# Performance work log

Measured on AMD Instinct MI355X. Metric: run time of the kernel, lower is better.

## Reference

```python
import jax, jax.numpy as jnp
import numpy as np
import math

INPUT_DIM = 256
HIDDEN_DIM = 128  # per-head dim
NUM_HEAD = 8
N = 1024          # seq len == variables
BATCH = 8
C = HIDDEN_DIM * NUM_HEAD  # 1024


def setup_inputs() -> dict:
    key = jax.random.key(0)
    ks = jax.random.split(key, 11)
    s = 0.02
    return {
        "x": jax.random.normal(ks[0], (BATCH, N, INPUT_DIM), dtype=jnp.float32),
        "B_bias": jax.random.normal(ks[1], (N, N), dtype=jnp.float32),
        "wq_w": jax.random.normal(ks[2], (INPUT_DIM, C), dtype=jnp.float32) * s,
        "wq_b": jax.random.normal(ks[3], (C,), dtype=jnp.float32) * s,
        "wk_w": jax.random.normal(ks[4], (INPUT_DIM, C), dtype=jnp.float32) * s,
        "wk_b": jax.random.normal(ks[5], (C,), dtype=jnp.float32) * s,
        "wv_w": jax.random.normal(ks[6], (INPUT_DIM, C), dtype=jnp.float32) * s,
        "wv_b": jax.random.normal(ks[7], (C,), dtype=jnp.float32) * s,
        "proj_w": jax.random.normal(ks[8], (C, HIDDEN_DIM), dtype=jnp.float32) * s,
        "proj_b": jax.random.normal(ks[9], (HIDDEN_DIM,), dtype=jnp.float32) * s,
    }


def reference(x, B_bias, wq_w, wq_b, wk_w, wk_b, wv_w, wv_b, proj_w, proj_b):
    B, n, _ = x.shape
    sdk = jnp.float32(math.sqrt(HIDDEN_DIM))
    # projections -> [B, N, C], split heads -> [B, H, N, h]
    def heads(y):
        return y.reshape(B, n, NUM_HEAD, HIDDEN_DIM).transpose(0, 2, 1, 3)
    q = heads(x @ wq_w + wq_b)
    k = heads(x @ wk_w + wk_b)
    v = heads(x @ wv_w + wv_b)
    # scores [B, H, N, N] with learned additive bias (broadcast over B, H)
    scores = jnp.einsum("bhnd,bhmd->bhnm", q, k) / sdk + B_bias
    attn = jax.nn.softmax(scores, axis=-1)
    out = jnp.einsum("bhnm,bhmd->bhnd", attn, v)  # [B, H, N, h]
    out = out.transpose(0, 2, 1, 3).reshape(B, n, C)
    return out @ proj_w + proj_b
```

## Files before the change

### kernel.cpp

```cpp
#include <hip/hip_runtime.h>
#include <math.h>

#define SEQ  1024
#define IND  256
#define CC   1024
#define NH   8
#define HD   128
#define BH   64

typedef __bf16 bf16x8 __attribute__((ext_vector_type(8)));
typedef __bf16 bf16x4 __attribute__((ext_vector_type(4)));
typedef float  f32x4  __attribute__((ext_vector_type(4)));
typedef unsigned short u16;

static constexpr float RSDK = 0.08838834764831845f;

__device__ __forceinline__ u16 f2bf(float f) {
    unsigned int u = __float_as_uint(f);
    u += 0x7fffu + ((u >> 16) & 1u);
    return (u16)(u >> 16);
}

__device__ __forceinline__ unsigned cvt_pk_bf16(float lo, float hi) {
    unsigned r;
    asm("v_cvt_pk_bf16_f32 %0, %1, %2" : "=v"(r) : "v"(lo), "v"(hi));
    return r;
}

__global__ __launch_bounds__(256) void prep_kernel(
    const float* __restrict__ x, u16* __restrict__ xb,
    const float* __restrict__ w0, const float* __restrict__ w1, const float* __restrict__ w2,
    u16* __restrict__ o0, u16* __restrict__ o1, u16* __restrict__ o2,
    const float* __restrict__ pw, u16* __restrict__ pT)
{
    __shared__ float tile[32][33];
    const int id = blockIdx.x;

    if (id < 2048) {
        const int i = id * 256 + threadIdx.x;
        float4 v = ((const float4*)x)[i];
        ushort4 o;
        o.x = f2bf(v.x); o.y = f2bf(v.y); o.z = f2bf(v.z); o.w = f2bf(v.w);
        ((ushort4*)xb)[i] = o;
        return;
    }

    const float* in; u16* out; int R, C, c0, r0;
    if (id < 2816) {
        const int rem = id - 2048;
        const int z = rem >> 8;
        const int rem2 = rem & 255;
        in  = (z == 0) ? w0 : (z == 1) ? w1 : w2;
        out = (z == 0) ? o0 : (z == 1) ? o1 : o2;
        R = IND; C = CC;
        c0 = (rem2 & 31) * 32;
        r0 = (rem2 >> 5) * 32;
    } else {
        const int rem = id - 2816;
        in = pw; out = pT;
        R = CC; C = HD;
        c0 = (rem & 3) * 32;
        r0 = (rem >> 2) * 32;
    }

    const int row = threadIdx.x >> 3, col4 = (threadIdx.x & 7) * 4;
    float4 v = *(const float4*)&in[(size_t)(r0 + row) * C + c0 + col4];
    tile[row][col4 + 0] = v.x; tile[row][col4 + 1] = v.y;
    tile[row][col4 + 2] = v.z; tile[row][col4 + 3] = v.w;
    __syncthreads();
    ushort4 o;
    o.x = f2bf(tile[col4 + 0][row]);
    o.y = f2bf(tile[col4 + 1][row]);
    o.z = f2bf(tile[col4 + 2][row]);
    o.w = f2bf(tile[col4 + 3][row]);
    *(ushort4*)&out[(size_t)(c0 + row) * R + r0 + col4] = o;
}

#define QKV_LDW 72
__global__ __launch_bounds__(256) void qkv_kernel(
    const u16* __restrict__ xb,
    const u16* __restrict__ wT0, const u16* __restrict__ wT1, const u16* __restrict__ wT2,
    const float* __restrict__ b0, const float* __restrict__ b1, const float* __restrict__ b2,
    u16* __restrict__ q_out, u16* __restrict__ k_out, u16* __restrict__ vt_out)
{
    const int mat = blockIdx.z;
    const u16* wT  = (mat == 0) ? wT0 : (mat == 1) ? wT1 : wT2;
    const float* wb = (mat == 0) ? b0 : (mat == 1) ? b1 : b2;
    const float scale = (mat == 0) ? RSDK : 1.0f;

    __shared__ __align__(16) u16 As[128 * QKV_LDW];
    __shared__ __align__(16) u16 Bs[128 * QKV_LDW];

    const int tid = threadIdx.x;
    const int lane = tid & 63, wave = tid >> 6;
    const int ln = lane & 15, quad = lane >> 4;
    const int m0 = blockIdx.x * 128;
    const int n0 = blockIdx.y * 128;
    const int wm = (wave & 1) * 64;
    const int wn = (wave >> 1) * 64;

    f32x4 acc[4][4];
    #pragma unroll
    for (int mb = 0; mb < 4; ++mb)
        #pragma unroll
        for (int nb = 0; nb < 4; ++nb)
            #pragma unroll
            for (int r = 0; r < 4; ++r) acc[mb][nb][r] = 0.0f;

    const int r8 = tid >> 3, pb8 = tid & 7;

    const u16* ag = xb + (size_t)(m0 + r8) * IND + pb8 * 8;
    const u16* bg = wT + (size_t)(n0 + r8) * IND + pb8 * 8;

    bf16x8 pa[4], pbv[4];
    #pragma unroll
    for (int c = 0; c < 4; ++c) {
        pa[c]  = *(const bf16x8*)(ag + (size_t)c * 32 * IND);
        pbv[c] = *(const bf16x8*)(bg + (size_t)c * 32 * IND);
    }

    for (int kt = 0; kt < 4; ++kt) {
        __syncthreads();
        #pragma unroll
        for (int c = 0; c < 4; ++c) {
            *(bf16x8*)(As + (size_t)(c * 32 + r8) * QKV_LDW + pb8 * 8) = pa[c];
            *(bf16x8*)(Bs + (size_t)(c * 32 + r8) * QKV_LDW + pb8 * 8) = pbv[c];
        }
        __syncthreads();
        if (kt < 3) {
            #pragma unroll
            for (int c = 0; c < 4; ++c) {
                pa[c]  = *(const bf16x8*)(ag + (size_t)c * 32 * IND + (kt + 1) * 64);
                pbv[c] = *(const bf16x8*)(bg + (size_t)c * 32 * IND + (kt + 1) * 64);
            }
        }
        #pragma unroll
        for (int ks = 0; ks < 2; ++ks) {
            bf16x8 af[4], bf[4];
            #pragma unroll
            for (int mb = 0; mb < 4; ++mb)
                af[mb] = *(const bf16x8*)(As + (size_t)(wm + mb * 16 + ln) * QKV_LDW
                                             + (ks * 4 + quad) * 8);
            #pragma unroll
            for (int nb = 0; nb < 4; ++nb)
                bf[nb] = *(const bf16x8*)(Bs + (size_t)(wn + nb * 16 + ln) * QKV_LDW
                                             + (ks * 4 + quad) * 8);
            #pragma unroll
            for (int mb = 0; mb < 4; ++mb)
                #pragma unroll
                for (int nb = 0; nb < 4; ++nb)
                    acc[mb][nb] = __builtin_amdgcn_mfma_f32_16x16x32_bf16(
                        af[mb], bf[nb], acc[mb][nb], 0, 0, 0);
        }
    }

    if (mat != 2) {
        u16* outp = (mat == 0) ? q_out : k_out;
        #pragma unroll
        for (int nb = 0; nb < 4; ++nb) {
            const int c = n0 + wn + nb * 16 + ln;
            const float bv = wb[c];
            const int h = c >> 7, d = c & 127;
            #pragma unroll
            for (int mb = 0; mb < 4; ++mb) {
                #pragma unroll
                for (int r = 0; r < 4; ++r) {
                    const int m = m0 + wm + mb * 16 + quad * 4 + r;
                    const int b = m >> 10, tok = m & 1023;
                    outp[((size_t)(b * NH + h) * SEQ + tok) * HD + d] =
                        f2bf((acc[mb][nb][r] + bv) * scale);
                }
            }
        }
    } else {
        #pragma unroll
        for (int nb = 0; nb < 4; ++nb) {
            const int c = n0 + wn + nb * 16 + ln;
            const float bv = wb[c];
            const int h = c >> 7, d = c & 127;
            #pragma unroll
            for (int mb = 0; mb < 4; ++mb) {
                const int m = m0 + wm + mb * 16 + quad * 4;
                const int b = m >> 10, tok0 = m & 1023;
                ushort4 o;
                o.x = f2bf(acc[mb][nb][0] + bv);
                o.y = f2bf(acc[mb][nb][1] + bv);
                o.z = f2bf(acc[mb][nb][2] + bv);
                o.w = f2bf(acc[mb][nb][3] + bv);
                *(ushort4*)&vt_out[((size_t)(b * NH + h) * HD + d) * SEQ + tok0] = o;
            }
        }
    }
}

#define KVB    32
#define KS_LDW 136
#define VS_LDW 40
__global__ __launch_bounds__(256, 4) void attn_kernel(
    const u16* __restrict__ Q, const u16* __restrict__ K,
    const u16* __restrict__ Vt, const float* __restrict__ bias,
    u16* __restrict__ aout)
{
    __shared__ __align__(16) u16 Ks[KVB * KS_LDW];
    __shared__ __align__(16) u16 Vs[128 * VS_LDW];

    const int tid = threadIdx.x;
    const int lane = tid & 63, wave = tid >> 6;
    const int ln = lane & 15, quad = lane >> 4;
    const int bh = blockIdx.x;
    const int q0 = blockIdx.y * 64 + wave * 16;

    bf16x8 qf[4];
    {
        const u16* qp = Q + ((size_t)bh * SEQ + q0 + ln) * HD + quad * 8;
        #pragma unroll
        for (int ks = 0; ks < 4; ++ks) qf[ks] = *(const bf16x8*)(qp + ks * 32);
    }

    f32x4 Oa[8];
    #pragma unroll
    for (int db = 0; db < 8; ++db)
        #pragma unroll
        for (int r = 0; r < 4; ++r) Oa[db][r] = 0.0f;
    float l_loc = 0.0f;

    const u16* Kg0 = K  + (size_t)bh * SEQ * HD;
    const u16* Vg0 = Vt + (size_t)bh * HD * SEQ;
    const float* brow = bias + (size_t)(q0 + ln) * SEQ + quad * 4;

    const int r16 = tid >> 4, pb16 = tid & 15;
    const int r4  = tid >> 2, pb4  = tid & 3;

    const u16* kg = Kg0 + (size_t)r16 * HD + pb16 * 8;
    const u16* vg = Vg0 + (size_t)r4 * SEQ + pb4 * 8;

    bf16x8 kp[2], vp[2];
    #pragma unroll
    for (int c = 0; c < 2; ++c) {
        kp[c] = *(const bf16x8*)(kg + (size_t)c * 16 * HD);
        vp[c] = *(const bf16x8*)(vg + (size_t)c * 64 * SEQ);
    }

    float4 bpre[2];
    #pragma unroll
    for (int nb = 0; nb < 2; ++nb)
        bpre[nb] = *(const float4*)(brow + nb * 16);

    for (int kt = 0; kt < 32; ++kt) {
        __syncthreads();
        #pragma unroll
        for (int c = 0; c < 2; ++c) {
            *(bf16x8*)(Ks + (size_t)(c * 16 + r16) * KS_LDW + pb16 * 8) = kp[c];
            *(bf16x8*)(Vs + (size_t)(c * 64 + r4) * VS_LDW + pb4 * 8)   = vp[c];
        }
        __syncthreads();

        if (kt < 31) {
            #pragma unroll
            for (int c = 0; c < 2; ++c) {
                kp[c] = *(const bf16x8*)(kg + (size_t)(kt + 1) * KVB * HD + (size_t)c * 16 * HD);
                vp[c] = *(const bf16x8*)(vg + (size_t)c * 64 * SEQ + (kt + 1) * KVB);
            }
        }

        float p8[2][4];
        #pragma unroll
        for (int nb = 0; nb < 2; ++nb) {
            const u16* kr = Ks + (size_t)(nb * 16 + ln) * KS_LDW;
            bf16x8 kf[4];
            #pragma unroll
            for (int ks = 0; ks < 4; ++ks)
                kf[ks] = *(const bf16x8*)(kr + (ks * 4 + quad) * 8);
            f32x4 s;
            #pragma unroll
            for (int r = 0; r < 4; ++r) s[r] = 0.0f;
            #pragma unroll
            for (int ks = 0; ks < 4; ++ks)
                s = __builtin_amdgcn_mfma_f32_16x16x32_bf16(kf[ks], qf[ks], s, 0, 0, 0);
            #pragma unroll
            for (int r = 0; r < 4; ++r) {
                const float p = __expf(s[r] + bpre[nb][r]);
                l_loc += p;
                p8[nb][r] = p;
            }
        }

        if (kt < 31) {
            #pragma unroll
            for (int nb = 0; nb < 2; ++nb)
                bpre[nb] = *(const float4*)(brow + (kt + 1) * KVB + nb * 16);
        }

        unsigned x0 = cvt_pk_bf16(p8[0][0], p8[0][1]);
        unsigned x1 = cvt_pk_bf16(p8[0][2], p8[0][3]);
        unsigned y0 = cvt_pk_bf16(p8[1][0], p8[1][1]);
        unsigned y1 = cvt_pk_bf16(p8[1][2], p8[1][3]);
        asm("v_permlane32_swap_b32 %0, %1" : "+v"(x0), "+v"(y0));
        asm("v_permlane32_swap_b32 %0, %1" : "+v"(x1), "+v"(y1));
        asm("v_permlane16_swap_b32 %0, %1" : "+v"(x0), "+v"(y0));
        asm("v_permlane16_swap_b32 %0, %1" : "+v"(x1), "+v"(y1));
        union { unsigned u[4]; bf16x8 v; } afu;
        afu.u[0] = x0; afu.u[1] = x1; afu.u[2] = y0; afu.u[3] = y1;
        const bf16x8 af = afu.v;

        #pragma unroll
        for (int db = 0; db < 8; ++db) {
            bf16x8 vf = *(const bf16x8*)(Vs + (size_t)(db * 16 + ln) * VS_LDW + quad * 8);
            Oa[db] = __builtin_amdgcn_mfma_f32_16x16x32_bf16(af, vf, Oa[db], 0, 0, 0);
        }
    }

    float ltot = l_loc;
    ltot += __shfl_xor(ltot, 16);
    ltot += __shfl_xor(ltot, 32);

    const int b = bh >> 3, h = bh & 7;
    #pragma unroll
    for (int r = 0; r < 4; ++r) {
        const float inv = 1.0f / __shfl(ltot, quad * 4 + r);
        const int tok = q0 + quad * 4 + r;
        u16* op = aout + ((size_t)(b * SEQ + tok)) * CC + h * HD + ln;
        #pragma unroll
        for (int db = 0; db < 8; ++db) op[db * 16] = f2bf(Oa[db][r] * inv);
    }
}

__global__ __launch_bounds__(256) void proj_kernel(
    const u16* __restrict__ A, const u16* __restrict__ pT,
    const float* __restrict__ pb, float* __restrict__ out)
{
    __shared__ float Rs[3][16 * 132];
    const int tid = threadIdx.x;
    const int lane = tid & 63, kh = tid >> 6;
    const int ln = lane & 15, quad = lane >> 4;
    const int m0 = blockIdx.x * 16;

    f32x4 acc[8];
    #pragma unroll
    for (int nb = 0; nb < 8; ++nb)
        #pragma unroll
        for (int r = 0; r < 4; ++r) acc[nb][r] = 0.0f;

    const u16* ap = A  + (size_t)(m0 + ln) * CC + kh * 256 + quad * 8;
    const u16* bp = pT + (size_t)ln * CC + kh * 256 + quad * 8;

    #pragma unroll
    for (int kt = 0; kt < 8; ++kt) {
        bf16x8 af = *(const bf16x8*)(ap + kt * 32);
        #pragma unroll
        for (int nb = 0; nb < 8; ++nb) {
            bf16x8 bf = *(const bf16x8*)(bp + (size_t)nb * 16 * CC + kt * 32);
            acc[nb] = __builtin_amdgcn_mfma_f32_16x16x32_bf16(af, bf, acc[nb], 0, 0, 0);
        }
    }

    if (kh > 0) {
        #pragma unroll
        for (int nb = 0; nb < 8; ++nb)
            #pragma unroll
            for (int r = 0; r < 4; ++r)
                Rs[kh - 1][(quad * 4 + r) * 132 + nb * 16 + ln] = acc[nb][r];
    }
    __syncthreads();
    if (kh == 0) {
        #pragma unroll
        for (int nb = 0; nb < 8; ++nb) {
            const int c = nb * 16 + ln;
            const float bv = pb[c];
            #pragma unroll
            for (int r = 0; r < 4; ++r) {
                const int ri = (quad * 4 + r) * 132 + c;
                out[(size_t)(m0 + quad * 4 + r) * HD + c] =
                    acc[nb][r] + Rs[0][ri] + Rs[1][ri] + Rs[2][ri] + bv;
            }
        }
    }
}

extern "C" void kernel_launch(void* const* d_in, const int* in_sizes, int n_in,
                              void* d_out, int out_size, void* d_ws, size_t ws_size,
                              hipStream_t stream)
{
    const float* x    = (const float*)d_in[0];
    const float* bias = (const float*)d_in[1];
    const float* wq   = (const float*)d_in[2];
    const float* wqb  = (const float*)d_in[3];
    const float* wk   = (const float*)d_in[4];
    const float* wkb  = (const float*)d_in[5];
    const float* wv   = (const float*)d_in[6];
    const float* wvb  = (const float*)d_in[7];
    const float* pw   = (const float*)d_in[8];
    const float* pb   = (const float*)d_in[9];
    float* out = (float*)d_out;

    u16* ws = (u16*)d_ws;
    size_t off = 0;
    u16* xb  = ws + off; off += (size_t)8192 * IND;
    u16* wqT = ws + off; off += (size_t)CC * IND;
    u16* wkT = ws + off; off += (size_t)CC * IND;
    u16* wvT = ws + off; off += (size_t)CC * IND;
    u16* pT  = ws + off; off += (size_t)HD * CC;
    u16* Qw  = ws + off; off += (size_t)BH * SEQ * HD;
    u16* Kw  = ws + off; off += (size_t)BH * SEQ * HD;
    u16* Vtw = ws + off; off += (size_t)BH * HD * SEQ;
    u16* Aw  = ws + off; off += (size_t)8192 * CC;

    prep_kernel<<<2944, 256, 0, stream>>>(x, xb, wq, wk, wv, wqT, wkT, wvT, pw, pT);
    qkv_kernel<<<dim3(64, 8, 3), 256, 0, stream>>>(
        xb, wqT, wkT, wvT, wqb, wkb, wvb, Qw, Kw, Vtw);
    attn_kernel<<<dim3(64, 16), 256, 0, stream>>>(Qw, Kw, Vtw, bias, Aw);
    proj_kernel<<<512, 256, 0, stream>>>(Aw, pT, pb, out);
}
```

Before: 181.8 us.

## Process two 16-row query tiles per wave in attention to reuse K/V fragments

Each wave now handles 32 query rows (two 16-row MFMA tiles) instead of 16, so every K fragment and V fragment read from LDS feeds two MFMAs. Each block covers 128 queries and the grid halves, which halves total K/V global-to-LDS traffic and the number of barrier iterations per query. The trade-off is doubled accumulator and Q registers, with launch bounds relaxed to 2 blocks per CU, plus fewer blocks (512) to spread across the GPU.

```diff
diff --git a/kernel.cpp b/kernel.cpp
--- a/kernel.cpp
+++ b/kernel.cpp
@@ -196,7 +196,7 @@
 #define KVB    32
 #define KS_LDW 136
 #define VS_LDW 40
-__global__ __launch_bounds__(256, 4) void attn_kernel(
+__global__ __launch_bounds__(256, 2) void attn_kernel(
     const u16* __restrict__ Q, const u16* __restrict__ K,
     const u16* __restrict__ Vt, const float* __restrict__ bias,
     u16* __restrict__ aout)
@@ -208,25 +208,29 @@
     const int lane = tid & 63, wave = tid >> 6;
     const int ln = lane & 15, quad = lane >> 4;
     const int bh = blockIdx.x;
-    const int q0 = blockIdx.y * 64 + wave * 16;
-
-    bf16x8 qf[4];
-    {
-        const u16* qp = Q + ((size_t)bh * SEQ + q0 + ln) * HD + quad * 8;
-        #pragma unroll
-        for (int ks = 0; ks < 4; ++ks) qf[ks] = *(const bf16x8*)(qp + ks * 32);
-    }
-
-    f32x4 Oa[8];
-    #pragma unroll
-    for (int db = 0; db < 8; ++db)
-        #pragma unroll
-        for (int r = 0; r < 4; ++r) Oa[db][r] = 0.0f;
-    float l_loc = 0.0f;
+    const int q0 = blockIdx.y * 128 + wave * 32;
+
+    bf16x8 qf[2][4];
+    #pragma unroll
+    for (int mb = 0; mb < 2; ++mb) {
+        const u16* qp = Q + ((size_t)bh * SEQ + q0 + mb * 16 + ln) * HD + quad * 8;
+        #pragma unroll
+        for (int ks = 0; ks < 4; ++ks) qf[mb][ks] = *(const bf16x8*)(qp + ks * 32);
+    }
+
+    f32x4 Oa[2][8];
+    #pragma unroll
+    for (int mb = 0; mb < 2; ++mb)
+        #pragma unroll
+        for (int db = 0; db < 8; ++db)
+            #pragma unroll
+            for (int r = 0; r < 4; ++r) Oa[mb][db][r] = 0.0f;
+    float l_loc[2] = {0.0f, 0.0f};
 
     const u16* Kg0 = K  + (size_t)bh * SEQ * HD;
     const u16* Vg0 = Vt + (size_t)bh * HD * SEQ;
-    const float* brow = bias + (size_t)(q0 + ln) * SEQ + quad * 4;
+    const float* brow0 = bias + (size_t)(q0 + ln) * SEQ + quad * 4;
+    const float* brow1 = brow0 + (size_t)16 * SEQ;
 
     const int r16 = tid >> 4, pb16 = tid & 15;
     const int r4  = tid >> 2, pb4  = tid & 3;
@@ -241,10 +245,12 @@
         vp[c] = *(const bf16x8*)(vg + (size_t)c * 64 * SEQ);
     }
 
-    float4 bpre[2];
-    #pragma unroll
-    for (int nb = 0; nb < 2; ++nb)
-        bpre[nb] = *(const float4*)(brow + nb * 16);
+    float4 bpre[2][2];
+    #pragma unroll
+    for (int mb = 0; mb < 2; ++mb)
+        #pragma unroll
+        for (int nb = 0; nb < 2; ++nb)
+            bpre[mb][nb] = *(const float4*)((mb ? brow1 : brow0) + nb * 16);
 
     for (int kt = 0; kt < 32; ++kt) {
         __syncthreads();
@@ -263,7 +269,7 @@
             }
         }
 
-        float p8[2][4];
+        float p8[2][2][4];
         #pragma unroll
         for (int nb = 0; nb < 2; ++nb) {
             const u16* kr = Ks + (size_t)(nb * 16 + ln) * KS_LDW;
@@ -271,57 +277,72 @@
             #pragma unroll
             for (int ks = 0; ks < 4; ++ks)
                 kf[ks] = *(const bf16x8*)(kr + (ks * 4 + quad) * 8);
-            f32x4 s;
-            #pragma unroll
-            for (int r = 0; r < 4; ++r) s[r] = 0.0f;
-            #pragma unroll
-            for (int ks = 0; ks < 4; ++ks)
-                s = __builtin_amdgcn_mfma_f32_16x16x32_bf16(kf[ks], qf[ks], s, 0, 0, 0);
-            #pragma unroll
-            for (int r = 0; r < 4; ++r) {
-                const float p = __expf(s[r] + bpre[nb][r]);
-                l_loc += p;
-                p8[nb][r] = p;
+            #pragma unroll
+            for (int mb = 0; mb < 2; ++mb) {
+                f32x4 s;
+                #pragma unroll
+                for (int r = 0; r < 4; ++r) s[r] = 0.0f;
+                #pragma unroll
+                for (int ks = 0; ks < 4; ++ks)
+                    s = __builtin_amdgcn_mfma_f32_16x16x32_bf16(kf[ks], qf[mb][ks], s, 0, 0, 0);
+                #pragma unroll
+                for (int r = 0; r < 4; ++r) {
+                    const float p = __expf(s[r] + bpre[mb][nb][r]);
+                    l_loc[mb] += p;
+                    p8[mb][nb][r] = p;
+                }
             }
         }
 
         if (kt < 31) {
             #pragma unroll
-            for (int nb = 0; nb < 2; ++nb)
-                bpre[nb] = *(const float4*)(brow + (kt + 1) * KVB + nb * 16);
-        }
-
-        unsigned x0 = cvt_pk_bf16(p8[0][0], p8[0][1]);
-        unsigned x1 = cvt_pk_bf16(p8[0][2], p8[0][3]);
-        unsigned y0 = cvt_pk_bf16(p8[1][0], p8[1][1]);
-        unsigned y1 = cvt_pk_bf16(p8[1][2], p8[1][3]);
-        asm("v_permlane32_swap_b32 %0, %1" : "+v"(x0), "+v"(y0));
-        asm("v_permlane32_swap_b32 %0, %1" : "+v"(x1), "+v"(y1));
-        asm("v_permlane16_swap_b32 %0, %1" : "+v"(x0), "+v"(y0));
-        asm("v_permlane16_swap_b32 %0, %1" : "+v"(x1), "+v"(y1));
-        union { unsigned u[4]; bf16x8 v; } afu;
-        afu.u[0] = x0; afu.u[1] = x1; afu.u[2] = y0; afu.u[3] = y1;
-        const bf16x8 af = afu.v;
+            for (int mb = 0; mb < 2; ++mb)
+                #pragma unroll
+                for (int nb = 0; nb < 2; ++nb)
+                    bpre[mb][nb] = *(const float4*)((mb ? brow1 : brow0)
+                                                    + (kt + 1) * KVB + nb * 16);
+        }
+
+        bf16x8 af[2];
+        #pragma unroll
+        for (int mb = 0; mb < 2; ++mb) {
+            unsigned x0 = cvt_pk_bf16(p8[mb][0][0], p8[mb][0][1]);
+            unsigned x1 = cvt_pk_bf16(p8[mb][0][2], p8[mb][0][3]);
+            unsigned y0 = cvt_pk_bf16(p8[mb][1][0], p8[mb][1][1]);
+            unsigned y1 = cvt_pk_bf16(p8[mb][1][2], p8[mb][1][3]);
+            asm("v_permlane32_swap_b32 %0, %1" : "+v"(x0), "+v"(y0));
+            asm("v_permlane32_swap_b32 %0, %1" : "+v"(x1), "+v"(y1));
+            asm("v_permlane16_swap_b32 %0, %1" : "+v"(x0), "+v"(y0));
+            asm("v_permlane16_swap_b32 %0, %1" : "+v"(x1), "+v"(y1));
+            union { unsigned u[4]; bf16x8 v; } afu;
+            afu.u[0] = x0; afu.u[1] = x1; afu.u[2] = y0; afu.u[3] = y1;
+            af[mb] = afu.v;
+        }
 
         #pragma unroll
         for (int db = 0; db < 8; ++db) {
             bf16x8 vf = *(const bf16x8*)(Vs + (size_t)(db * 16 + ln) * VS_LDW + quad * 8);
-            Oa[db] = __builtin_amdgcn_mfma_f32_16x16x32_bf16(af, vf, Oa[db], 0, 0, 0);
-        }
-    }
-
-    float ltot = l_loc;
-    ltot += __shfl_xor(ltot, 16);
-    ltot += __shfl_xor(ltot, 32);
+            #pragma unroll
+            for (int mb = 0; mb < 2; ++mb)
+                Oa[mb][db] = __builtin_amdgcn_mfma_f32_16x16x32_bf16(
+                    af[mb], vf, Oa[mb][db], 0, 0, 0);
+        }
+    }
 
     const int b = bh >> 3, h = bh & 7;
     #pragma unroll
-    for (int r = 0; r < 4; ++r) {
-        const float inv = 1.0f / __shfl(ltot, quad * 4 + r);
-        const int tok = q0 + quad * 4 + r;
-        u16* op = aout + ((size_t)(b * SEQ + tok)) * CC + h * HD + ln;
-        #pragma unroll
-        for (int db = 0; db < 8; ++db) op[db * 16] = f2bf(Oa[db][r] * inv);
+    for (int mb = 0; mb < 2; ++mb) {
+        float ltot = l_loc[mb];
+        ltot += __shfl_xor(ltot, 16);
+        ltot += __shfl_xor(ltot, 32);
+        #pragma unroll
+        for (int r = 0; r < 4; ++r) {
+            const float inv = 1.0f / __shfl(ltot, quad * 4 + r);
+            const int tok = q0 + mb * 16 + quad * 4 + r;
+            u16* op = aout + ((size_t)(b * SEQ + tok)) * CC + h * HD + ln;
+            #pragma unroll
+            for (int db = 0; db < 8; ++db) op[db * 16] = f2bf(Oa[mb][db][r] * inv);
+        }
     }
 }
 
@@ -408,6 +429,6 @@
     prep_kernel<<<2944, 256, 0, stream>>>(x, xb, wq, wk, wv, wqT, wkT, wvT, pw, pT);
     qkv_kernel<<<dim3(64, 8, 3), 256, 0, stream>>>(
         xb, wqT, wkT, wvT, wqb, wkb, wvb, Qw, Kw, Vtw);
-    attn_kernel<<<dim3(64, 16), 256, 0, stream>>>(Qw, Kw, Vtw, bias, Aw);
+    attn_kernel<<<dim3(64, 8), 256, 0, stream>>>(Qw, Kw, Vtw, bias, Aw);
     proj_kernel<<<512, 256, 0, stream>>>(Aw, pT, pb, out);
 }
```

Result: faster. 172.1 us (-5.4%).
